# Kernel tuning notes

Measured on AMD Instinct MI355X. Metric: run time of the kernel, lower is better.

The kernel has to match this reference:

```python
import jax, jax.numpy as jnp
import numpy as np

B, S, D = 4, 2048, 1024
H, DK, DV = 16, 64, 64


def setup_inputs() -> dict:
    key = jax.random.key(0)
    ks = jax.random.split(key, 12)
    scale = 1.0 / np.sqrt(D)
    queries = jax.random.normal(ks[0], (B, S, D), dtype=jnp.float32)
    keys_ = jax.random.normal(ks[1], (B, S, D), dtype=jnp.float32)
    values = jax.random.normal(ks[2], (B, S, D), dtype=jnp.float32)
    # binary additive mask (1 = masked out), broadcastable over batch and heads
    mask = jax.random.randint(ks[3], (1, 1, S, S), 0, 2).astype(jnp.float32)
    Wq = jax.random.normal(ks[4], (D, H * DK), dtype=jnp.float32) * scale
    bq = jnp.zeros((H * DK,), dtype=jnp.float32)
    Wk = jax.random.normal(ks[5], (D, H * DK), dtype=jnp.float32) * scale
    bk = jnp.zeros((H * DK,), dtype=jnp.float32)
    Wv = jax.random.normal(ks[6], (D, H * DV), dtype=jnp.float32) * scale
    bv = jnp.zeros((H * DV,), dtype=jnp.float32)
    Wo = jax.random.normal(ks[7], (H * DV, D), dtype=jnp.float32) * scale
    bo = jnp.zeros((D,), dtype=jnp.float32)
    return {"queries": queries, "keys": keys_, "values": values, "mask": mask,
            "Wq": Wq, "bq": bq, "Wk": Wk, "bk": bk, "Wv": Wv, "bv": bv,
            "Wo": Wo, "bo": bo}


def reference(queries, keys, values, mask, Wq, bq, Wk, bk, Wv, bv, Wo, bo):
    b = queries.shape[0]
    # projections + split heads: [B, S, H*Dh] -> [B, H, S, Dh]
    q = (queries @ Wq + bq).reshape(b, -1, H, DK).transpose(0, 2, 1, 3)
    k = (keys @ Wk + bk).reshape(b, -1, H, DK).transpose(0, 2, 1, 3)
    v = (values @ Wv + bv).reshape(b, -1, H, DV).transpose(0, 2, 1, 3)
    scores = jnp.einsum("bhqd,bhkd->bhqk", q, k) / jnp.sqrt(jnp.float32(DK))
    scores = scores + mask * (-1e9)
    attn = jax.nn.softmax(scores, axis=-1)
    ctx = jnp.einsum("bhqk,bhkd->bhqd", attn, v)  # [B, H, S, DV]
    ctx = ctx.transpose(0, 2, 1, 3).reshape(b, -1, H * DV)
    return ctx @ Wo + bo
```

## Files before the change

### kernel.cpp

```cpp
#include <hip/hip_runtime.h>
#include <cstdint>
#include <cstddef>

typedef __attribute__((ext_vector_type(8))) short bf16x8;
typedef __attribute__((ext_vector_type(4))) short bf16x4;
typedef __attribute__((ext_vector_type(4))) float f32x4;

__device__ __forceinline__ unsigned short f2bf(float f) {
    union { float f; unsigned int u; } v; v.f = f;
    unsigned int r = v.u + 0x7FFFu + ((v.u >> 16) & 1u);
    return (unsigned short)(r >> 16);
}
__device__ __forceinline__ unsigned int pk2(float a, float b) {
    return (unsigned int)f2bf(a) | ((unsigned int)f2bf(b) << 16);
}
__device__ __forceinline__ unsigned int pkpair(float a, float b) {
#if __has_builtin(__builtin_amdgcn_cvt_pk_bf16_f32)
    auto r = __builtin_amdgcn_cvt_pk_bf16_f32(a, b);
    return __builtin_bit_cast(unsigned int, r);
#else
    unsigned int ua = __builtin_bit_cast(unsigned int, a) + 0x8000u;
    unsigned int ub = __builtin_bit_cast(unsigned int, b) + 0x8000u;
    return __builtin_amdgcn_perm(ub, ua, 0x07060302u);
#endif
}

typedef __attribute__((address_space(1))) void gvoid;
typedef __attribute__((address_space(3))) void svoid;
__device__ __forceinline__ void ld16_lds(const void* g, void* l) {
    __builtin_amdgcn_global_load_lds((gvoid*)g, (svoid*)l, 16, 0, 0);
}

#define QSCALE 0.1803368801111204f

__global__ __launch_bounds__(256)
void preprocess(const float* __restrict__ Qin, const float* __restrict__ Kin,
                const float* __restrict__ Vin, const float* __restrict__ Msk,
                const float* __restrict__ Wq, const float* __restrict__ Wk,
                const float* __restrict__ Wv, const float* __restrict__ Wo,
                unsigned short* __restrict__ acts, unsigned short* __restrict__ m16,
                unsigned short* __restrict__ wts)
{
    __shared__ float t[32][33];
    const int bx = blockIdx.x, tid = threadIdx.x;
    if (bx < 12288) {
        const int which = bx >> 12;
        const float* src = (which == 0) ? Qin : (which == 1) ? Kin : Vin;
        unsigned short* dst = acts + ((size_t)which << 23);
        const size_t i = ((size_t)(bx & 4095) * 256 + tid) * 8;
        float4 a = *(const float4*)(src + i);
        float4 b = *(const float4*)(src + i + 4);
        uint4 p;
        p.x = pk2(a.x, a.y); p.y = pk2(a.z, a.w);
        p.z = pk2(b.x, b.y); p.w = pk2(b.z, b.w);
        *(uint4*)(dst + i) = p;
    } else if (bx < 14336) {
        const int row = bx - 12288;
        const int k0 = tid * 8;
        const float* src = Msk + (size_t)row * 2048 + k0;
        float4 a = *(const float4*)src;
        float4 b = *(const float4*)(src + 4);
        unsigned int m0 = (a.x != 0.f) ? 0u : 0xFFFFu;
        unsigned int m1 = (a.y != 0.f) ? 0u : 0xFFFFu;
        unsigned int m2 = (a.z != 0.f) ? 0u : 0xFFFFu;
        unsigned int m3 = (a.w != 0.f) ? 0u : 0xFFFFu;
        unsigned int m4 = (b.x != 0.f) ? 0u : 0xFFFFu;
        unsigned int m5 = (b.y != 0.f) ? 0u : 0xFFFFu;
        unsigned int m6 = (b.z != 0.f) ? 0u : 0xFFFFu;
        unsigned int m7 = (b.w != 0.f) ? 0u : 0xFFFFu;
        const int kt = k0 >> 6, mt = (k0 >> 4) & 3, q0 = (k0 >> 2) & 3;
        uint2 A; A.x = m0 | (m1 << 16); A.y = m2 | (m3 << 16);
        uint2 B; B.x = m4 | (m5 << 16); B.y = m6 | (m7 << 16);
        const size_t baseA = ((size_t)(kt * 4 + q0    ) * 2048 + row) * 16 + mt * 4;
        const size_t baseB = ((size_t)(kt * 4 + q0 + 1) * 2048 + row) * 16 + mt * 4;
        *(uint2*)(m16 + baseA) = A;
        *(uint2*)(m16 + baseB) = B;
    } else {
        const int idx = bx - 14336;
        const int z = idx >> 10, rem = idx & 1023;
        const float* W = (z == 0) ? Wq : (z == 1) ? Wk : (z == 2) ? Wv : Wo;
        unsigned short* Wt = wts + ((size_t)z << 20);
        const int n0 = (rem & 31) << 5, k0 = (rem >> 5) << 5;
        const int tx = tid & 31, ty = tid >> 5;
#pragma unroll
        for (int i = 0; i < 4; i++)
            t[ty + 8 * i][tx] = W[(size_t)(k0 + ty + 8 * i) * 1024 + n0 + tx];
        __syncthreads();
#pragma unroll
        for (int i = 0; i < 4; i++)
            Wt[(size_t)(n0 + ty + 8 * i) * 1024 + k0 + tx] = f2bf(t[tx][ty + 8 * i]);
    }
}

__global__ __launch_bounds__(256, 4)
void qkv_gemm(const unsigned short* __restrict__ A0,
              const unsigned short* __restrict__ W0,
              const float* __restrict__ bq, const float* __restrict__ bk,
              const float* __restrict__ bv,
              unsigned short* __restrict__ out0)
{
    __shared__ __align__(16) unsigned short sm[18432];

    const int z = blockIdx.z;
    const unsigned short* A  = A0 + ((size_t)z << 23);
    const unsigned short* Wt = W0 + ((size_t)z << 20);
    const float* bias = (z == 0) ? bq : (z == 1) ? bk : bv;
    unsigned short* ob = out0 + ((size_t)z << 23);

    const int tid = threadIdx.x, lane = tid & 63, wave = tid >> 6;
    const int quad = lane >> 4, l16 = lane & 15;
    const int wr = wave >> 1, wc = wave & 1;
    const int m0 = blockIdx.x * 128, n0 = blockIdx.y * 128;

    const char* Ab = (const char*)A  + (size_t)m0 * 2048;
    const char* Bb = (const char*)Wt + (size_t)n0 * 2048;
    const int sr0 = tid >> 2, sc0 = (tid & 3) << 4;

    f32x4 acc[4][4];
#pragma unroll
    for (int i = 0; i < 4; i++)
#pragma unroll
        for (int j = 0; j < 4; j++) acc[i][j] = (f32x4){0.f, 0.f, 0.f, 0.f};

    {
        char* Ad = (char*)sm;
        char* Bd = Ad + 8192;
        ld16_lds(Ab + (size_t)sr0 * 2048 + sc0,        Ad + tid * 16);
        ld16_lds(Ab + (size_t)(sr0 + 64) * 2048 + sc0, Ad + (256 + tid) * 16);
        ld16_lds(Bb + (size_t)sr0 * 2048 + sc0,        Bd + tid * 16);
        ld16_lds(Bb + (size_t)(sr0 + 64) * 2048 + sc0, Bd + (256 + tid) * 16);
    }

    for (int it = 0; it < 32; ++it) {
        const int cur = it & 1;
        __syncthreads();
        if (it < 31) {
            const int kb2 = (it + 1) * 64;
            char* Ad = (char*)(sm + (cur ^ 1) * 8192);
            char* Bd = Ad + 8192;
            ld16_lds(Ab + (size_t)sr0 * 2048 + kb2 + sc0,        Ad + tid * 16);
            ld16_lds(Ab + (size_t)(sr0 + 64) * 2048 + kb2 + sc0, Ad + (256 + tid) * 16);
            ld16_lds(Bb + (size_t)sr0 * 2048 + kb2 + sc0,        Bd + tid * 16);
            ld16_lds(Bb + (size_t)(sr0 + 64) * 2048 + kb2 + sc0, Bd + (256 + tid) * 16);
        }
        const unsigned short* As = sm + cur * 8192;
        const unsigned short* Bs = As + 4096;

        bf16x8 af[4], bfr[4];
#pragma unroll
        for (int mt = 0; mt < 4; mt++)
            af[mt] = *(const bf16x8*)&As[(wr * 64 + mt * 16 + l16) * 32 + quad * 8];
#pragma unroll
        for (int nt = 0; nt < 4; nt++)
            bfr[nt] = *(const bf16x8*)&Bs[(wc * 64 + nt * 16 + l16) * 32 + quad * 8];
#pragma unroll
        for (int mt = 0; mt < 4; mt++)
#pragma unroll
            for (int nt = 0; nt < 4; nt++)
                acc[mt][nt] = __builtin_amdgcn_mfma_f32_16x16x32_bf16(af[mt], bfr[nt], acc[mt][nt], 0, 0, 0);
    }

    float bvv[4];
#pragma unroll
    for (int nt = 0; nt < 4; nt++) bvv[nt] = bias[n0 + wc * 64 + nt * 16 + l16];

    if (z < 2) {
        __syncthreads();
        unsigned short* T = sm;
#pragma unroll
        for (int mt = 0; mt < 4; mt++) {
            const int row = wr * 64 + mt * 16 + quad * 4;
#pragma unroll
            for (int nt = 0; nt < 4; nt++) {
                const int col = wc * 64 + nt * 16 + l16;
#pragma unroll
                for (int r = 0; r < 4; r++) {
                    float o = acc[mt][nt][r] + bvv[nt];
                    if (z == 0) o *= QSCALE;
                    T[(row + r) * 132 + col] = f2bf(o);
                }
            }
        }
        __syncthreads();
#pragma unroll
        for (int j = 0; j < 8; j++) {
            const int id = j * 256 + tid;
            const int row = id >> 4, cc = id & 15;
            const uint2 v01 = *(const uint2*)&T[row * 132 + cc * 8];
            const uint2 v23 = *(const uint2*)&T[row * 132 + cc * 8 + 4];
            uint4 v; v.x = v01.x; v.y = v01.y; v.z = v23.x; v.w = v23.y;
            const int mg = m0 + row;
            const int b = mg >> 11, s = mg & 2047;
            const int ng = n0 + cc * 8;
            const int h = ng >> 6, dk = ng & 63;
            *(uint4*)&ob[((size_t)((b << 4) + h) * 2048 + s) * 64 + dk] = v;
        }
    } else {
        __syncthreads();
        unsigned short* T = sm + wave * (64 * 72);
#pragma unroll
        for (int mt = 0; mt < 4; mt++)
#pragma unroll
            for (int nt = 0; nt < 4; nt++)
#pragma unroll
                for (int r = 0; r < 4; r++)
                    T[(nt * 16 + l16) * 72 + mt * 16 + quad * 4 + r] = f2bf(acc[mt][nt][r] + bvv[nt]);
        __syncthreads();
#pragma unroll
        for (int i = 0; i < 8; i++) {
            const int nl = i * 8 + (lane >> 3);
            const int mc = lane & 7;
            uint4 v = *(const uint4*)&T[nl * 72 + mc * 8];
            const int n  = n0 + wc * 64 + nl;
            const int mg = m0 + wr * 64 + mc * 8;
            const int b = mg >> 11, s = mg & 2047;
            const int h = n >> 6, dv = n & 63;
            *(uint4*)&ob[((size_t)((b << 4) + h) * 64 + dv) * 2048 + s] = v;
        }
    }
}

__global__ __launch_bounds__(256, 3)
void gemm_final(const unsigned short* __restrict__ A,
                const unsigned short* __restrict__ Wt, const float* __restrict__ bias,
                float* __restrict__ of)
{
    __shared__ __align__(16) unsigned short sm[16384];

    const int tid = threadIdx.x, lane = tid & 63, wave = tid >> 6;
    const int quad = lane >> 4, l16 = lane & 15;
    const int wr = wave >> 1, wc = wave & 1;
    const int m0 = blockIdx.x * 128, n0 = blockIdx.y * 128;

    const char* Ab = (const char*)A  + (size_t)m0 * 2048;
    const char* Bb = (const char*)Wt + (size_t)n0 * 2048;
    const int sr0 = tid >> 2, sc0 = (tid & 3) << 4;

    f32x4 acc[4][4];
#pragma unroll
    for (int i = 0; i < 4; i++)
#pragma unroll
        for (int j = 0; j < 4; j++) acc[i][j] = (f32x4){0.f, 0.f, 0.f, 0.f};

    {
        char* Ad = (char*)sm;
        char* Bd = Ad + 8192;
        ld16_lds(Ab + (size_t)sr0 * 2048 + sc0,        Ad + tid * 16);
        ld16_lds(Ab + (size_t)(sr0 + 64) * 2048 + sc0, Ad + (256 + tid) * 16);
        ld16_lds(Bb + (size_t)sr0 * 2048 + sc0,        Bd + tid * 16);
        ld16_lds(Bb + (size_t)(sr0 + 64) * 2048 + sc0, Bd + (256 + tid) * 16);
    }

    for (int it = 0; it < 32; ++it) {
        const int cur = it & 1;
        __syncthreads();
        if (it < 31) {
            const int kb2 = (it + 1) * 64;
            char* Ad = (char*)(sm + (cur ^ 1) * 8192);
            char* Bd = Ad + 8192;
            ld16_lds(Ab + (size_t)sr0 * 2048 + kb2 + sc0,        Ad + tid * 16);
            ld16_lds(Ab + (size_t)(sr0 + 64) * 2048 + kb2 + sc0, Ad + (256 + tid) * 16);
            ld16_lds(Bb + (size_t)sr0 * 2048 + kb2 + sc0,        Bd + tid * 16);
            ld16_lds(Bb + (size_t)(sr0 + 64) * 2048 + kb2 + sc0, Bd + (256 + tid) * 16);
        }
        const unsigned short* As = sm + cur * 8192;
        const unsigned short* Bs = As + 4096;

        bf16x8 af[4], bfr[4];
#pragma unroll
        for (int mt = 0; mt < 4; mt++)
            af[mt] = *(const bf16x8*)&As[(wr * 64 + mt * 16 + l16) * 32 + quad * 8];
#pragma unroll
        for (int nt = 0; nt < 4; nt++)
            bfr[nt] = *(const bf16x8*)&Bs[(wc * 64 + nt * 16 + l16) * 32 + quad * 8];
#pragma unroll
        for (int mt = 0; mt < 4; mt++)
#pragma unroll
            for (int nt = 0; nt < 4; nt++)
                acc[mt][nt] = __builtin_amdgcn_mfma_f32_16x16x32_bf16(af[mt], bfr[nt], acc[mt][nt], 0, 0, 0);
    }

    float bvv[4];
#pragma unroll
    for (int nt = 0; nt < 4; nt++) bvv[nt] = bias[n0 + wc * 64 + nt * 16 + l16];
#pragma unroll
    for (int mt = 0; mt < 4; mt++) {
        const int m = m0 + wr * 64 + mt * 16 + quad * 4;
#pragma unroll
        for (int nt = 0; nt < 4; nt++) {
            const int n = n0 + wc * 64 + nt * 16 + l16;
#pragma unroll
            for (int r = 0; r < 4; r++)
                of[(size_t)(m + r) * 1024 + n] = acc[mt][nt][r] + bvv[nt];
        }
    }
}

__global__ __launch_bounds__(256, 4)
void attn_kernel(const unsigned short* __restrict__ q,
                 const unsigned short* __restrict__ k,
                 const unsigned short* __restrict__ vT,
                 const unsigned short* __restrict__ m16,
                 unsigned short* __restrict__ ctx)
{
    __shared__ __align__(16) unsigned short Ks[2][64 * 64];
    __shared__ __align__(16) unsigned short Vs[2][64 * 64];

    const int tid = threadIdx.x, lane = tid & 63, wave = tid >> 6;
    const int quad = lane >> 4, l16 = lane & 15;
    const int sw = l16 & 7;
    const int bid = blockIdx.x;
    const int qblk = bid & 15, h = (bid >> 4) & 15, b = bid >> 8;

    const unsigned short* qb = q  + (size_t)(b * 16 + h) * 2048 * 64;
    const unsigned short* kb = k  + (size_t)(b * 16 + h) * 2048 * 64;
    const unsigned short* vb = vT + (size_t)(b * 16 + h) * 64 * 2048;

    const int c0 = tid, c1 = 256 + tid;
    const int r0 = c0 >> 3, gcc0 = (c0 & 7) ^ (r0 & 7);
    const int r1 = c1 >> 3, gcc1 = (c1 & 7) ^ (r1 & 7);

    int qrow[2];
    bf16x8 qf[2][2];
    f32x4 O0[4], O1[4];
    f32x4 lacc0 = (f32x4){0.f,0.f,0.f,0.f}, lacc1 = (f32x4){0.f,0.f,0.f,0.f};
    const bf16x4 vones = (bf16x4){(short)0x3F80, (short)0x3F80, (short)0x3F80, (short)0x3F80};
#pragma unroll
    for (int g = 0; g < 2; g++) {
        qrow[g] = qblk * 128 + wave * 32 + g * 16 + l16;
        qf[g][0] = *(const bf16x8*)&qb[qrow[g] * 64 + quad * 8];
        qf[g][1] = *(const bf16x8*)&qb[qrow[g] * 64 + 32 + quad * 8];
    }
#pragma unroll
    for (int i = 0; i < 4; i++) { O0[i] = (f32x4){0.f,0.f,0.f,0.f}; O1[i] = (f32x4){0.f,0.f,0.f,0.f}; }
    const unsigned short* mq0 = m16 + ((size_t)quad * 2048 + qrow[0]) * 16;
    const unsigned short* mq1 = m16 + ((size_t)quad * 2048 + qrow[1]) * 16;
    const size_t mstep = (size_t)4 * 2048 * 16;

    {
        ld16_lds((const char*)kb + (size_t)r0 * 128 + gcc0 * 16, (char*)Ks[0] + c0 * 16);
        ld16_lds((const char*)kb + (size_t)r1 * 128 + gcc1 * 16, (char*)Ks[0] + c1 * 16);
        ld16_lds((const char*)vb + (size_t)r0 * 4096 + gcc0 * 16, (char*)Vs[0] + c0 * 16);
        ld16_lds((const char*)vb + (size_t)r1 * 4096 + gcc1 * 16, (char*)Vs[0] + c1 * 16);
    }

    for (int it = 0; it < 32; ++it) {
        const int kt = it << 6;
        const int cur = it & 1, nxt = cur ^ 1;
        __syncthreads();

        const uint4 lo0 = *(const uint4*)(mq0);
        const uint4 hi0 = *(const uint4*)(mq0 + 8);
        const uint4 lo1 = *(const uint4*)(mq1);
        const uint4 hi1 = *(const uint4*)(mq1 + 8);
        mq0 += mstep; mq1 += mstep;

        if (it < 31) {
            const char* kg = (const char*)kb + (size_t)(kt + 64) * 128;
            const char* vg = (const char*)vb + (size_t)(kt + 64) * 2;
            ld16_lds(kg + (size_t)r0 * 128 + gcc0 * 16, (char*)Ks[nxt] + c0 * 16);
            ld16_lds(kg + (size_t)r1 * 128 + gcc1 * 16, (char*)Ks[nxt] + c1 * 16);
            ld16_lds(vg + (size_t)r0 * 4096 + gcc0 * 16, (char*)Vs[nxt] + c0 * 16);
            ld16_lds(vg + (size_t)r1 * 4096 + gcc1 * 16, (char*)Vs[nxt] + c1 * 16);
        }

        const unsigned short* Kc = Ks[cur];
        const unsigned short* Vc = Vs[cur];

        f32x4 S0[4], S1[4];
        __builtin_amdgcn_s_setprio(1);
#pragma unroll
        for (int mt = 0; mt < 4; mt++) {
            const unsigned short* kp = Kc + (mt * 16 + l16) * 64;
            bf16x8 ka0 = *(const bf16x8*)&kp[((quad    ) ^ sw) * 8];
            bf16x8 ka1 = *(const bf16x8*)&kp[((4 + quad) ^ sw) * 8];
            f32x4 z0 = (f32x4){0.f,0.f,0.f,0.f};
            f32x4 z1 = (f32x4){0.f,0.f,0.f,0.f};
            z0 = __builtin_amdgcn_mfma_f32_16x16x32_bf16(ka0, qf[0][0], z0, 0, 0, 0);
            S0[mt] = __builtin_amdgcn_mfma_f32_16x16x32_bf16(ka1, qf[0][1], z0, 0, 0, 0);
            z1 = __builtin_amdgcn_mfma_f32_16x16x32_bf16(ka0, qf[1][0], z1, 0, 0, 0);
            S1[mt] = __builtin_amdgcn_mfma_f32_16x16x32_bf16(ka1, qf[1][1], z1, 0, 0, 0);
        }
        __builtin_amdgcn_s_setprio(0);
        bf16x4 pf0[4], pf1[4];
#pragma unroll
        for (int mt = 0; mt < 4; mt++) {
            const unsigned int ax0 = (mt == 0) ? lo0.x : (mt == 1) ? lo0.z : (mt == 2) ? hi0.x : hi0.z;
            const unsigned int ay0 = (mt == 0) ? lo0.y : (mt == 1) ? lo0.w : (mt == 2) ? hi0.y : hi0.w;
            const unsigned int ax1 = (mt == 0) ? lo1.x : (mt == 1) ? lo1.z : (mt == 2) ? hi1.x : hi1.z;
            const unsigned int ay1 = (mt == 0) ? lo1.y : (mt == 1) ? lo1.w : (mt == 2) ? hi1.y : hi1.w;
            float p0[4], p1[4];
#pragma unroll
            for (int r = 0; r < 4; r++) {
                p0[r] = __builtin_amdgcn_exp2f(S0[mt][r]);
                p1[r] = __builtin_amdgcn_exp2f(S1[mt][r]);
            }
            uint2 u0, u1;
            u0.x = pkpair(p0[0], p0[1]) & ax0;
            u0.y = pkpair(p0[2], p0[3]) & ay0;
            u1.x = pkpair(p1[0], p1[1]) & ax1;
            u1.y = pkpair(p1[2], p1[3]) & ay1;
            pf0[mt] = __builtin_bit_cast(bf16x4, u0);
            pf1[mt] = __builtin_bit_cast(bf16x4, u1);
        }
        __builtin_amdgcn_s_setprio(1);
#pragma unroll
        for (int mt = 0; mt < 4; mt++) {
            lacc0 = __builtin_amdgcn_mfma_f32_16x16x16bf16_1k(vones, pf0[mt], lacc0, 0, 0, 0);
            lacc1 = __builtin_amdgcn_mfma_f32_16x16x16bf16_1k(vones, pf1[mt], lacc1, 0, 0, 0);
        }
#pragma unroll
        for (int dvt = 0; dvt < 4; dvt++) {
            const unsigned short* vp = Vc + (dvt * 16 + l16) * 64;
#pragma unroll
            for (int mt = 0; mt < 4; mt++) {
                uint2 vv = *(const uint2*)&vp[((2 * mt + (quad >> 1)) ^ sw) * 8 + (quad & 1) * 4];
                bf16x4 va = __builtin_bit_cast(bf16x4, vv);
                O0[dvt] = __builtin_amdgcn_mfma_f32_16x16x16bf16_1k(va, pf0[mt], O0[dvt], 0, 0, 0);
                O1[dvt] = __builtin_amdgcn_mfma_f32_16x16x16bf16_1k(va, pf1[mt], O1[dvt], 0, 0, 0);
            }
        }
        __builtin_amdgcn_s_setprio(0);
    }
#pragma unroll
    for (int g = 0; g < 2; g++) {
        const float rl = __builtin_amdgcn_rcpf(g ? lacc1[0] : lacc0[0]);
        const f32x4* O = g ? O1 : O0;
#pragma unroll
        for (int dvt = 0; dvt < 4; dvt++) {
            uint2 st;
            st.x = pk2(O[dvt][0] * rl, O[dvt][1] * rl);
            st.y = pk2(O[dvt][2] * rl, O[dvt][3] * rl);
            *(uint2*)&ctx[(size_t)(b * 2048 + qrow[g]) * 1024 + h * 64 + dvt * 16 + quad * 4] = st;
        }
    }
}

extern "C" void kernel_launch(void* const* d_in, const int* in_sizes, int n_in,
                              void* d_out, int out_size, void* d_ws, size_t ws_size,
                              hipStream_t stream)
{
    const float* Qin = (const float*)d_in[0];
    const float* Kin = (const float*)d_in[1];
    const float* Vin = (const float*)d_in[2];
    const float* Msk = (const float*)d_in[3];
    const float* Wq  = (const float*)d_in[4];
    const float* bq  = (const float*)d_in[5];
    const float* Wk  = (const float*)d_in[6];
    const float* bk  = (const float*)d_in[7];
    const float* Wv  = (const float*)d_in[8];
    const float* bv  = (const float*)d_in[9];
    const float* Wo  = (const float*)d_in[10];
    const float* bo  = (const float*)d_in[11];

    unsigned short* w = (unsigned short*)d_ws;
    unsigned short* wts  = w;
    unsigned short* wto  = w + 3u * (1u << 20);
    unsigned short* qcv  = w + 4u * (1u << 20);
    unsigned short* qb   = qcv + 3u * (1u << 23);
    unsigned short* kb   = qb  + (1u << 23);
    unsigned short* vTb  = kb  + (1u << 23);
    unsigned short* ctxb = qcv;
    unsigned short* m16  = vTb + (1u << 23);

    preprocess<<<18432, 256, 0, stream>>>(Qin, Kin, Vin, Msk, Wq, Wk, Wv, Wo,
                                          qcv, m16, wts);
    qkv_gemm<<<dim3(64, 8, 3), 256, 0, stream>>>(qcv, wts, bq, bk, bv, qb);
    attn_kernel<<<1024, 256, 0, stream>>>(qb, kb, vTb, m16, ctxb);
    gemm_final<<<dim3(64, 8), 256, 0, stream>>>(ctxb, wto, bo, (float*)d_out);
}
```

Measured before the change: 375.6 us.

## Triple-buffer LDS loads in QKV and output GEMMs with explicit vmcnt waits

Both projection GEMMs move from a double-buffered to a triple-buffered LDS pipeline, issuing global-to-LDS loads two k-tiles ahead. Partial s_waitcnt vmcnt counts let loads stay in flight across iterations instead of draining fully each step, hiding more global latency. The cost is 48KB of LDS per block, which lowers the QKV kernel's occupancy hint from 4 to 3 blocks, and a second barrier per iteration.

Measured after the change: 373.5 us. No clear change (-0.6%).

```diff
diff --git a/kernel.cpp b/kernel.cpp
--- a/kernel.cpp
+++ b/kernel.cpp
@@ -92,14 +92,14 @@
     }
 }
 
-__global__ __launch_bounds__(256, 4)
+__global__ __launch_bounds__(256, 3)
 void qkv_gemm(const unsigned short* __restrict__ A0,
               const unsigned short* __restrict__ W0,
               const float* __restrict__ bq, const float* __restrict__ bk,
               const float* __restrict__ bv,
               unsigned short* __restrict__ out0)
 {
-    __shared__ __align__(16) unsigned short sm[18432];
+    __shared__ __align__(16) unsigned short sm[24576];
 
     const int z = blockIdx.z;
     const unsigned short* A  = A0 + ((size_t)z << 23);
@@ -122,27 +122,31 @@
 #pragma unroll
         for (int j = 0; j < 4; j++) acc[i][j] = (f32x4){0.f, 0.f, 0.f, 0.f};
 
-    {
-        char* Ad = (char*)sm;
-        char* Bd = Ad + 8192;
-        ld16_lds(Ab + (size_t)sr0 * 2048 + sc0,        Ad + tid * 16);
-        ld16_lds(Ab + (size_t)(sr0 + 64) * 2048 + sc0, Ad + (256 + tid) * 16);
-        ld16_lds(Bb + (size_t)sr0 * 2048 + sc0,        Bd + tid * 16);
-        ld16_lds(Bb + (size_t)(sr0 + 64) * 2048 + sc0, Bd + (256 + tid) * 16);
-    }
+#define QKV_STAGE(KT, BUF)                                                       \
+    {                                                                            \
+        char* Ad = (char*)(sm + (BUF) * 8192);                                   \
+        char* Bd = Ad + 8192;                                                    \
+        const int kb2 = (KT) * 64;                                               \
+        ld16_lds(Ab + (size_t)sr0 * 2048 + kb2 + sc0,        Ad + tid * 16);     \
+        ld16_lds(Ab + (size_t)(sr0 + 64) * 2048 + kb2 + sc0, Ad + (256 + tid) * 16); \
+        ld16_lds(Bb + (size_t)sr0 * 2048 + kb2 + sc0,        Bd + tid * 16);     \
+        ld16_lds(Bb + (size_t)(sr0 + 64) * 2048 + kb2 + sc0, Bd + (256 + tid) * 16); \
+    }
+
+    QKV_STAGE(0, 0)
+    QKV_STAGE(1, 1)
 
     for (int it = 0; it < 32; ++it) {
-        const int cur = it & 1;
-        __syncthreads();
-        if (it < 31) {
-            const int kb2 = (it + 1) * 64;
-            char* Ad = (char*)(sm + (cur ^ 1) * 8192);
-            char* Bd = Ad + 8192;
-            ld16_lds(Ab + (size_t)sr0 * 2048 + kb2 + sc0,        Ad + tid * 16);
-            ld16_lds(Ab + (size_t)(sr0 + 64) * 2048 + kb2 + sc0, Ad + (256 + tid) * 16);
-            ld16_lds(Bb + (size_t)sr0 * 2048 + kb2 + sc0,        Bd + tid * 16);
-            ld16_lds(Bb + (size_t)(sr0 + 64) * 2048 + kb2 + sc0, Bd + (256 + tid) * 16);
-        }
+        const int cur = it % 3;
+        asm volatile("" ::: "memory");
+        __builtin_amdgcn_s_barrier();
+        if (it < 30) QKV_STAGE(it + 2, (it + 2) % 3)
+        if (it < 30)       asm volatile("s_waitcnt vmcnt(8)" ::: "memory");
+        else if (it == 30) asm volatile("s_waitcnt vmcnt(4)" ::: "memory");
+        else               asm volatile("s_waitcnt vmcnt(0)" ::: "memory");
+        __builtin_amdgcn_s_barrier();
+        asm volatile("" ::: "memory");
+
         const unsigned short* As = sm + cur * 8192;
         const unsigned short* Bs = As + 4096;
 
@@ -218,6 +222,7 @@
             *(uint4*)&ob[((size_t)((b << 4) + h) * 64 + dv) * 2048 + s] = v;
         }
     }
+#undef QKV_STAGE
 }
 
 __global__ __launch_bounds__(256, 3)
@@ -225,7 +230,7 @@
                 const unsigned short* __restrict__ Wt, const float* __restrict__ bias,
                 float* __restrict__ of)
 {
-    __shared__ __align__(16) unsigned short sm[16384];
+    __shared__ __align__(16) unsigned short sm[24576];
 
     const int tid = threadIdx.x, lane = tid & 63, wave = tid >> 6;
     const int quad = lane >> 4, l16 = lane & 15;
@@ -242,27 +247,31 @@
 #pragma unroll
         for (int j = 0; j < 4; j++) acc[i][j] = (f32x4){0.f, 0.f, 0.f, 0.f};
 
-    {
-        char* Ad = (char*)sm;
-        char* Bd = Ad + 8192;
-        ld16_lds(Ab + (size_t)sr0 * 2048 + sc0,        Ad + tid * 16);
-        ld16_lds(Ab + (size_t)(sr0 + 64) * 2048 + sc0, Ad + (256 + tid) * 16);
-        ld16_lds(Bb + (size_t)sr0 * 2048 + sc0,        Bd + tid * 16);
-        ld16_lds(Bb + (size_t)(sr0 + 64) * 2048 + sc0, Bd + (256 + tid) * 16);
-    }
+#define FIN_STAGE(KT, BUF)                                                       \
+    {                                                                            \
+        char* Ad = (char*)(sm + (BUF) * 8192);                                   \
+        char* Bd = Ad + 8192;                                                    \
+        const int kb2 = (KT) * 64;                                               \
+        ld16_lds(Ab + (size_t)sr0 * 2048 + kb2 + sc0,        Ad + tid * 16);     \
+        ld16_lds(Ab + (size_t)(sr0 + 64) * 2048 + kb2 + sc0, Ad + (256 + tid) * 16); \
+        ld16_lds(Bb + (size_t)sr0 * 2048 + kb2 + sc0,        Bd + tid * 16);     \
+        ld16_lds(Bb + (size_t)(sr0 + 64) * 2048 + kb2 + sc0, Bd + (256 + tid) * 16); \
+    }
+
+    FIN_STAGE(0, 0)
+    FIN_STAGE(1, 1)
 
     for (int it = 0; it < 32; ++it) {
-        const int cur = it & 1;
-        __syncthreads();
-        if (it < 31) {
-            const int kb2 = (it + 1) * 64;
-            char* Ad = (char*)(sm + (cur ^ 1) * 8192);
-            char* Bd = Ad + 8192;
-            ld16_lds(Ab + (size_t)sr0 * 2048 + kb2 + sc0,        Ad + tid * 16);
-            ld16_lds(Ab + (size_t)(sr0 + 64) * 2048 + kb2 + sc0, Ad + (256 + tid) * 16);
-            ld16_lds(Bb + (size_t)sr0 * 2048 + kb2 + sc0,        Bd + tid * 16);
-            ld16_lds(Bb + (size_t)(sr0 + 64) * 2048 + kb2 + sc0, Bd + (256 + tid) * 16);
-        }
+        const int cur = it % 3;
+        asm volatile("" ::: "memory");
+        __builtin_amdgcn_s_barrier();
+        if (it < 30) FIN_STAGE(it + 2, (it + 2) % 3)
+        if (it < 30)       asm volatile("s_waitcnt vmcnt(8)" ::: "memory");
+        else if (it == 30) asm volatile("s_waitcnt vmcnt(4)" ::: "memory");
+        else               asm volatile("s_waitcnt vmcnt(0)" ::: "memory");
+        __builtin_amdgcn_s_barrier();
+        asm volatile("" ::: "memory");
+
         const unsigned short* As = sm + cur * 8192;
         const unsigned short* Bs = As + 4096;
 
@@ -294,6 +303,7 @@
                 of[(size_t)(m + r) * 1024 + n] = acc[mt][nt][r] + bvv[nt];
         }
     }
+#undef FIN_STAGE
 }
 
 __global__ __launch_bounds__(256, 4)
```
